# Optimization experiments

Measured on AMD Instinct MI355X. Metric: run time of the kernel, lower is better.

Reference implementation:

```python
import jax, jax.numpy as jnp
import numpy as np

# ---- static configuration (matches init_kwargs / input_specs) ----
B, N = 4, 128            # images, proposals per image
C = 256                  # feature channels (in_channels)
HF, WF = 23, 30          # feature map size (input 736x960 / 32)
PH, PW = 7, 7            # pooled_size
SCALE = 1.0 / 32.0       # scale_factor
HIMG, WIMG = HF * 32, WF * 32
KH = HF // PH + 2        # max rows any pooling bin can span
KW = WF // PW + 2        # max cols any pooling bin can span
HID, OUT = 256, 5
NEG = -1e30


def _roi_pool_one(f, box):
    """Quantized ROI max pooling for one proposal.
    f: (C, HF, WF) feature map; box: (4,) [x1,y1,x2,y2] in feature coords.
    Returns (C, PH, PW)."""
    box = jax.lax.stop_gradient(box)  # indices are non-differentiable
    x1 = jnp.clip(jnp.floor(box[0]).astype(jnp.int32), 0, WF - 1)
    y1 = jnp.clip(jnp.floor(box[1]).astype(jnp.int32), 0, HF - 1)
    roi_w = jnp.clip(jnp.ceil(box[2]).astype(jnp.int32) - x1, 1, WF)
    roi_h = jnp.clip(jnp.ceil(box[3]).astype(jnp.int32) - y1, 1, HF)
    ph = jnp.arange(PH)
    pw = jnp.arange(PW)
    hs = y1 + (ph * roi_h) // PH                       # bin row starts (PH,)
    he = y1 + ((ph + 1) * roi_h + PH - 1) // PH        # bin row ends (ceil)
    ws = x1 + (pw * roi_w) // PW
    we = x1 + ((pw + 1) * roi_w + PW - 1) // PW
    hidx = hs[:, None] + jnp.arange(KH)[None, :]       # (PH, KH)
    hval = (hidx < he[:, None]) & (hidx < HF)
    widx = ws[:, None] + jnp.arange(KW)[None, :]       # (PW, KW)
    wval = (widx < we[:, None]) & (widx < WF)
    rows = f[:, jnp.clip(hidx, 0, HF - 1), :]          # (C, PH, KH, WF) gather
    rmax = jnp.max(jnp.where(hval[None, :, :, None], rows, NEG), axis=2)  # (C, PH, WF)
    cols = rmax[:, :, jnp.clip(widx, 0, WF - 1)]       # (C, PH, PW, KW) gather
    return jnp.max(jnp.where(wval[None, None], cols, NEG), axis=3)        # (C, PH, PW)


# vmap over proposals, then over images: (B,C,HF,WF),(B,N,4) -> (B,N,C,PH,PW)
_roi_pool = jax.vmap(jax.vmap(_roi_pool_one, in_axes=(None, 0)), in_axes=(0, 0))


def setup_inputs() -> dict:
    key = jax.random.key(0)
    ks = jax.random.split(key, 8)
    features = jax.random.normal(ks[0], (B, C, HF, WF), jnp.float32)
    # valid proposals in image coordinates (min box side ~32 px)
    x1 = jax.random.uniform(ks[1], (B, N)) * (WIMG - 32.0)
    y1 = jax.random.uniform(ks[2], (B, N)) * (HIMG - 32.0)
    x2 = x1 + 32.0 + jax.random.uniform(ks[3], (B, N)) * (WIMG - 32.0 - x1)
    y2 = y1 + 32.0 + jax.random.uniform(ks[4], (B, N)) * (HIMG - 32.0 - y1)
    conf = jax.random.normal(ks[5], (B, N))
    proposals = jnp.stack([x1, y1, x2, y2, conf], axis=-1)  # (B, N, 5)
    W1 = jax.random.normal(ks[6], (HID, C * PH * PW), jnp.float32) * 0.01
    b1 = jnp.zeros((HID,), jnp.float32)
    W2 = jax.random.normal(ks[7], (OUT, HID), jnp.float32) * 0.01
    b2 = jnp.zeros((OUT,), jnp.float32)
    return {"features": features, "proposals": proposals,
            "W1": W1, "b1": b1, "W2": W2, "b2": b2}


def reference(features, proposals, W1, b1, W2, b2):
    boxes_feat = proposals[..., :4] * SCALE                 # image -> feature coords
    pooled = _roi_pool(features, boxes_feat)                # (B, N, C, PH, PW)
    flat = pooled.reshape(B, N, C * PH * PW)
    h = jax.nn.relu(jnp.einsum('bnf,hf->bnh', flat, W1) + b1)
    out = jnp.einsum('bnh,oh->bno', h, W2) + b2             # (B, N, 5)
    refined_boxes = proposals[..., :4] + out[..., :4]
    refined_conf = jax.nn.sigmoid(proposals[..., 4:5] + out[..., 4:5])
    return jnp.concatenate([refined_boxes, refined_conf], axis=-1)  # (B, N, 5)
```

## Files before the change

### kernel.cpp

```cpp
#include <hip/hip_runtime.h>
#include <math.h>

#define Bq 4
#define Nq 128
#define Cq 256
#define HFq 23
#define WFq 30
#define PHq 7
#define PWq 7
#define HIDq 256
#define OUTq 5
#define Fq (Cq*PHq*PWq)
#define Mq (Bq*Nq)
#define HWq (HFq*WFq)
#define SCALEq (1.0f/32.0f)
#define NEGq (-1e30f)
#define KHq 5
#define KWq 6
#define SPLITK 14
#define KCH (Fq/SPLITK)
#define KSTEPS (KCH/32)

typedef float f32x4 __attribute__((ext_vector_type(4)));
typedef __bf16 bf16x8 __attribute__((ext_vector_type(8)));

__device__ __forceinline__ unsigned short f2b(float f) {
    unsigned int u = __float_as_uint(f);
    unsigned int r = (u + 0x7FFFu + ((u >> 16) & 1u)) >> 16;
    return (unsigned short)r;
}

__global__ __launch_bounds__(256) void k_transpose(const float* __restrict__ feat,
                                                   float* __restrict__ ft) {
    __shared__ float t[32][33];
    int bb = blockIdx.z;
    const float* src = feat + (size_t)bb * Cq * HWq;
    float* dst = ft + (size_t)bb * HWq * Cq;
    int x0 = blockIdx.x * 32;
    int c0 = blockIdx.y * 32;
    int tx = threadIdx.x, ty = threadIdx.y;
#pragma unroll
    for (int i = 0; i < 4; ++i) {
        int c = c0 + ty + i * 8;
        int x = x0 + tx;
        if (x < HWq) t[ty + i * 8][tx] = src[(size_t)c * HWq + x];
    }
    __syncthreads();
#pragma unroll
    for (int i = 0; i < 4; ++i) {
        int x = x0 + ty + i * 8;
        int c = c0 + tx;
        if (x < HWq) dst[(size_t)x * Cq + c] = t[tx][ty + i * 8];
    }
}

__global__ __launch_bounds__(256) void k_w1perm(const float* __restrict__ W1,
                                                unsigned short* __restrict__ w1p) {
    __shared__ __align__(16) unsigned short s[Fq];
    int j = blockIdx.x;
    const float4* src = (const float4*)(W1 + (size_t)j * Fq);
    for (int i = threadIdx.x; i < Fq / 4; i += 256) {
        float4 v = src[i];
        ushort4 o;
        o.x = f2b(v.x); o.y = f2b(v.y); o.z = f2b(v.z); o.w = f2b(v.w);
        ((ushort4*)s)[i] = o;
    }
    __syncthreads();
    uint4* dst = (uint4*)(w1p + (size_t)j * Fq);
    for (int i = threadIdx.x; i < Fq / 8; i += 256) {
        int base = i * 8;
        int cell = base >> 8;
        int c0 = base & 255;
        unsigned short tmp[8];
#pragma unroll
        for (int u = 0; u < 8; ++u) tmp[u] = s[(c0 + u) * 49 + cell];
        dst[i] = *(const uint4*)tmp;
    }
}

__global__ __launch_bounds__(256) void k_pool(const float* __restrict__ ft,
                                              const float* __restrict__ props,
                                              unsigned short* __restrict__ pooled) {
    int wave = threadIdx.x >> 6;
    int lane = threadIdx.x & 63;
    int g = blockIdx.y * 4 + wave;
    int m = blockIdx.x;
    int b = m >> 7;
    const float* pr = props + (size_t)m * 5;
    float b0 = pr[0] * SCALEq, b1v = pr[1] * SCALEq;
    float b2v = pr[2] * SCALEq, b3v = pr[3] * SCALEq;
    int x1 = min(max((int)floorf(b0), 0), WFq - 1);
    int y1 = min(max((int)floorf(b1v), 0), HFq - 1);
    int rw = min(max((int)ceilf(b2v) - x1, 1), WFq);
    int rh = min(max((int)ceilf(b3v) - y1, 1), HFq);
    const float* ftb = ft + (size_t)b * HWq * Cq + lane * 4;
    unsigned short* pm = pooled + (size_t)m * Fq + lane * 4;

    for (int cell = g; cell < PHq * PWq; cell += 8) {
        int ph = cell / 7;
        int pw = cell - ph * 7;
        int hs = y1 + (ph * rh) / PHq;
        int he = min(y1 + ((ph + 1) * rh + PHq - 1) / PHq, HFq);
        int ws = x1 + (pw * rw) / PWq;
        int we = min(x1 + ((pw + 1) * rw + PWq - 1) / PWq, WFq);
        f32x4 acc = {NEGq, NEGq, NEGq, NEGq};
#pragma unroll
        for (int kh = 0; kh < KHq; ++kh) {
            if (hs + kh < he) {
                const float* rowp = ftb + (size_t)((hs + kh) * WFq) * Cq;
#pragma unroll
                for (int kw = 0; kw < KWq; ++kw) {
                    if (ws + kw < we) {
                        f32x4 v = *(const f32x4*)(rowp + (size_t)(ws + kw) * Cq);
                        acc.x = fmaxf(acc.x, v.x);
                        acc.y = fmaxf(acc.y, v.y);
                        acc.z = fmaxf(acc.z, v.z);
                        acc.w = fmaxf(acc.w, v.w);
                    }
                }
            }
        }
        ushort4 o;
        o.x = f2b(acc.x); o.y = f2b(acc.y); o.z = f2b(acc.z); o.w = f2b(acc.w);
        *(ushort4*)(pm + (size_t)cell * Cq) = o;
    }
}

__global__ __launch_bounds__(256) void k_gemm1(const unsigned short* __restrict__ pooled,
                                               const unsigned short* __restrict__ w1p,
                                               float* __restrict__ part) {
    __shared__ __align__(16) unsigned short As[64 * 32];
    __shared__ __align__(16) unsigned short Bs[64 * 32];
    int m0 = blockIdx.x * 64;
    int j0 = blockIdx.y * 64;
    int kz = blockIdx.z;
    int tid = threadIdx.x;
    int r = tid >> 2, qq = tid & 3;
    const uint4* ap = (const uint4*)(pooled + (size_t)(m0 + r) * Fq + (size_t)kz * KCH + qq * 8);
    const uint4* bp = (const uint4*)(w1p + (size_t)(j0 + r) * Fq + (size_t)kz * KCH + qq * 8);
    int lane = tid & 63, wv = tid >> 6;
    int q = lane >> 4, mr = lane & 15;
    f32x4 acc0 = {0.f, 0.f, 0.f, 0.f};
    f32x4 acc1 = {0.f, 0.f, 0.f, 0.f};
    f32x4 acc2 = {0.f, 0.f, 0.f, 0.f};
    f32x4 acc3 = {0.f, 0.f, 0.f, 0.f};
    const bf16x8* afp = (const bf16x8*)(As + (wv * 16 + mr) * 32 + q * 8);
    const bf16x8* bfp0 = (const bf16x8*)(Bs + (0 + mr) * 32 + q * 8);
    const bf16x8* bfp1 = (const bf16x8*)(Bs + (16 + mr) * 32 + q * 8);
    const bf16x8* bfp2 = (const bf16x8*)(Bs + (32 + mr) * 32 + q * 8);
    const bf16x8* bfp3 = (const bf16x8*)(Bs + (48 + mr) * 32 + q * 8);
    uint4* asw = (uint4*)(As + r * 32 + qq * 8);
    uint4* bsw = (uint4*)(Bs + r * 32 + qq * 8);
    uint4 av = ap[0];
    uint4 bv = bp[0];
    for (int s = 0; s < KSTEPS; ++s) {
        __syncthreads();
        *asw = av;
        *bsw = bv;
        __syncthreads();
        if (s + 1 < KSTEPS) {
            av = ap[(s + 1) * 4];
            bv = bp[(s + 1) * 4];
        }
        bf16x8 a = *afp;
        acc0 = __builtin_amdgcn_mfma_f32_16x16x32_bf16(a, *bfp0, acc0, 0, 0, 0);
        acc1 = __builtin_amdgcn_mfma_f32_16x16x32_bf16(a, *bfp1, acc1, 0, 0, 0);
        acc2 = __builtin_amdgcn_mfma_f32_16x16x32_bf16(a, *bfp2, acc2, 0, 0, 0);
        acc3 = __builtin_amdgcn_mfma_f32_16x16x32_bf16(a, *bfp3, acc3, 0, 0, 0);
    }
    float* pbase = part + (size_t)kz * Mq * HIDq;
    int mb = m0 + wv * 16 + q * 4;
    int jj = j0 + mr;
#pragma unroll
    for (int r2 = 0; r2 < 4; ++r2) {
        float* row = pbase + (size_t)(mb + r2) * HIDq + jj;
        row[0]  = acc0[r2];
        row[16] = acc1[r2];
        row[32] = acc2[r2];
        row[48] = acc3[r2];
    }
}

__global__ __launch_bounds__(256) void k_reduce(const float* __restrict__ part,
                                                const float* __restrict__ b1,
                                                float* __restrict__ h) {
    int m = blockIdx.x, j = threadIdx.x;
    float s = 0.f;
#pragma unroll
    for (int z = 0; z < SPLITK; ++z) s += part[((size_t)z * Mq + m) * HIDq + j];
    s += b1[j];
    h[(size_t)m * HIDq + j] = fmaxf(s, 0.f);
}

__global__ __launch_bounds__(256) void k_final(const float* __restrict__ h,
                                               const float* __restrict__ W2,
                                               const float* __restrict__ b2,
                                               const float* __restrict__ props,
                                               float* __restrict__ out) {
    __shared__ float red[OUTq][4];
    int m = blockIdx.x, j = threadIdx.x;
    float hv = h[(size_t)m * HIDq + j];
    float p[OUTq];
#pragma unroll
    for (int o = 0; o < OUTq; ++o) p[o] = hv * W2[(size_t)o * HIDq + j];
    int lane = j & 63, wid = j >> 6;
#pragma unroll
    for (int o = 0; o < OUTq; ++o) {
        float v = p[o];
        v += __shfl_xor(v, 1);
        v += __shfl_xor(v, 2);
        v += __shfl_xor(v, 4);
        v += __shfl_xor(v, 8);
        v += __shfl_xor(v, 16);
        v += __shfl_xor(v, 32);
        if (lane == 0) red[o][wid] = v;
    }
    __syncthreads();
    if (j < OUTq) {
        float s = red[j][0] + red[j][1] + red[j][2] + red[j][3] + b2[j];
        float pv = props[(size_t)m * 5 + j];
        float r;
        if (j < 4) r = pv + s;
        else r = 1.f / (1.f + expf(-(pv + s)));
        out[(size_t)m * 5 + j] = r;
    }
}

extern "C" void kernel_launch(void* const* d_in, const int* in_sizes, int n_in,
                              void* d_out, int out_size, void* d_ws, size_t ws_size,
                              hipStream_t stream) {
    const float* feat  = (const float*)d_in[0];
    const float* props = (const float*)d_in[1];
    const float* W1    = (const float*)d_in[2];
    const float* b1    = (const float*)d_in[3];
    const float* W2    = (const float*)d_in[4];
    const float* b2    = (const float*)d_in[5];
    float* out = (float*)d_out;

    char* ws = (char*)d_ws;
    float* ft              = (float*)(ws);
    unsigned short* w1p    = (unsigned short*)(ws + 2826240);
    unsigned short* pooled = (unsigned short*)(ws + 9248768);
    float* part            = (float*)(ws + 22093824);
    float* h               = (float*)(ws + 29433856);

    k_transpose<<<dim3(22, 8, 4), dim3(32, 8), 0, stream>>>(feat, ft);
    k_w1perm<<<HIDq, 256, 0, stream>>>(W1, w1p);
    k_pool<<<dim3(Mq, 2), 256, 0, stream>>>(ft, props, pooled);
    k_gemm1<<<dim3(8, 4, SPLITK), 256, 0, stream>>>(pooled, w1p, part);
    k_reduce<<<Mq, 256, 0, stream>>>(part, b1, h);
    k_final<<<Mq, 256, 0, stream>>>(h, W2, b2, props, out);
}
```

Baseline: 128.7 us.

## Fuse all stages into one cooperative persistent kernel with grid syncs

Replaces the six separate kernel launches (transpose, W1 permute, pool, split-K GEMM, reduce, final) with a single cooperative kernel of 256 blocks that runs each stage in turn and separates them with grid-wide syncs. The split-K factor drops from 14 to 8 so the GEMM tile count matches the 256-block grid, and the reduce and final stages are merged so the h buffer is no longer written. This removes launch overhead and intermediate round-trips. In exchange each stage is limited to 256 blocks, which lowers parallelism in the pool stage, and each grid sync has its own cost.

```diff
diff --git a/kernel.cpp b/kernel.cpp
--- a/kernel.cpp
+++ b/kernel.cpp
@@ -1,5 +1,8 @@
 #include <hip/hip_runtime.h>
+#include <hip/hip_cooperative_groups.h>
 #include <math.h>
+
+namespace cg = cooperative_groups;
 
 #define Bq 4
 #define Nq 128
@@ -17,7 +20,7 @@
 #define NEGq (-1e30f)
 #define KHq 5
 #define KWq 6
-#define SPLITK 14
+#define SPLITK 8
 #define KCH (Fq/SPLITK)
 #define KSTEPS (KCH/32)
 
@@ -30,199 +33,209 @@
     return (unsigned short)r;
 }
 
-__global__ __launch_bounds__(256) void k_transpose(const float* __restrict__ feat,
-                                                   float* __restrict__ ft) {
-    __shared__ float t[32][33];
-    int bb = blockIdx.z;
-    const float* src = feat + (size_t)bb * Cq * HWq;
-    float* dst = ft + (size_t)bb * HWq * Cq;
-    int x0 = blockIdx.x * 32;
-    int c0 = blockIdx.y * 32;
-    int tx = threadIdx.x, ty = threadIdx.y;
-#pragma unroll
-    for (int i = 0; i < 4; ++i) {
-        int c = c0 + ty + i * 8;
-        int x = x0 + tx;
-        if (x < HWq) t[ty + i * 8][tx] = src[(size_t)c * HWq + x];
-    }
-    __syncthreads();
-#pragma unroll
-    for (int i = 0; i < 4; ++i) {
-        int x = x0 + ty + i * 8;
-        int c = c0 + tx;
-        if (x < HWq) dst[(size_t)x * Cq + c] = t[tx][ty + i * 8];
-    }
-}
-
-__global__ __launch_bounds__(256) void k_w1perm(const float* __restrict__ W1,
-                                                unsigned short* __restrict__ w1p) {
-    __shared__ __align__(16) unsigned short s[Fq];
-    int j = blockIdx.x;
-    const float4* src = (const float4*)(W1 + (size_t)j * Fq);
-    for (int i = threadIdx.x; i < Fq / 4; i += 256) {
-        float4 v = src[i];
-        ushort4 o;
-        o.x = f2b(v.x); o.y = f2b(v.y); o.z = f2b(v.z); o.w = f2b(v.w);
-        ((ushort4*)s)[i] = o;
-    }
-    __syncthreads();
-    uint4* dst = (uint4*)(w1p + (size_t)j * Fq);
-    for (int i = threadIdx.x; i < Fq / 8; i += 256) {
-        int base = i * 8;
-        int cell = base >> 8;
-        int c0 = base & 255;
-        unsigned short tmp[8];
-#pragma unroll
-        for (int u = 0; u < 8; ++u) tmp[u] = s[(c0 + u) * 49 + cell];
-        dst[i] = *(const uint4*)tmp;
-    }
-}
-
-__global__ __launch_bounds__(256) void k_pool(const float* __restrict__ ft,
-                                              const float* __restrict__ props,
-                                              unsigned short* __restrict__ pooled) {
-    int wave = threadIdx.x >> 6;
-    int lane = threadIdx.x & 63;
-    int g = blockIdx.y * 4 + wave;
-    int m = blockIdx.x;
-    int b = m >> 7;
-    const float* pr = props + (size_t)m * 5;
-    float b0 = pr[0] * SCALEq, b1v = pr[1] * SCALEq;
-    float b2v = pr[2] * SCALEq, b3v = pr[3] * SCALEq;
-    int x1 = min(max((int)floorf(b0), 0), WFq - 1);
-    int y1 = min(max((int)floorf(b1v), 0), HFq - 1);
-    int rw = min(max((int)ceilf(b2v) - x1, 1), WFq);
-    int rh = min(max((int)ceilf(b3v) - y1, 1), HFq);
-    const float* ftb = ft + (size_t)b * HWq * Cq + lane * 4;
-    unsigned short* pm = pooled + (size_t)m * Fq + lane * 4;
-
-    for (int cell = g; cell < PHq * PWq; cell += 8) {
-        int ph = cell / 7;
-        int pw = cell - ph * 7;
-        int hs = y1 + (ph * rh) / PHq;
-        int he = min(y1 + ((ph + 1) * rh + PHq - 1) / PHq, HFq);
-        int ws = x1 + (pw * rw) / PWq;
-        int we = min(x1 + ((pw + 1) * rw + PWq - 1) / PWq, WFq);
-        f32x4 acc = {NEGq, NEGq, NEGq, NEGq};
-#pragma unroll
-        for (int kh = 0; kh < KHq; ++kh) {
-            if (hs + kh < he) {
-                const float* rowp = ftb + (size_t)((hs + kh) * WFq) * Cq;
-#pragma unroll
-                for (int kw = 0; kw < KWq; ++kw) {
-                    if (ws + kw < we) {
-                        f32x4 v = *(const f32x4*)(rowp + (size_t)(ws + kw) * Cq);
-                        acc.x = fmaxf(acc.x, v.x);
-                        acc.y = fmaxf(acc.y, v.y);
-                        acc.z = fmaxf(acc.z, v.z);
-                        acc.w = fmaxf(acc.w, v.w);
+union SMem {
+    float t[32][33];
+    unsigned short s[Fq];
+    struct { unsigned short A[64 * 32]; unsigned short B[64 * 32]; } g;
+    float red[OUTq][4];
+};
+
+__global__ __launch_bounds__(256) void k_fused(const float* __restrict__ feat,
+                                               const float* __restrict__ props,
+                                               const float* __restrict__ W1,
+                                               const float* __restrict__ b1,
+                                               const float* __restrict__ W2,
+                                               const float* __restrict__ b2,
+                                               float* __restrict__ out,
+                                               float* __restrict__ ft,
+                                               unsigned short* __restrict__ w1p,
+                                               unsigned short* __restrict__ pooled,
+                                               float* __restrict__ part) {
+    cg::grid_group grid = cg::this_grid();
+    __shared__ __align__(16) SMem sm;
+    int tid = threadIdx.x;
+    int bid = blockIdx.x;
+
+    {
+        int tx = tid & 31, ty = tid >> 5;
+        for (int job = bid; job < 704; job += 256) {
+            int bb = job / 176;
+            int rem = job - bb * 176;
+            int cblk = rem / 22;
+            int xblk = rem - cblk * 22;
+            const float* src = feat + (size_t)bb * Cq * HWq;
+            float* dst = ft + (size_t)bb * HWq * Cq;
+            int x0 = xblk * 32, c0 = cblk * 32;
+#pragma unroll
+            for (int i = 0; i < 4; ++i) {
+                int c = c0 + ty + i * 8, x = x0 + tx;
+                if (x < HWq) sm.t[ty + i * 8][tx] = src[(size_t)c * HWq + x];
+            }
+            __syncthreads();
+#pragma unroll
+            for (int i = 0; i < 4; ++i) {
+                int x = x0 + ty + i * 8, c = c0 + tx;
+                if (x < HWq) dst[(size_t)x * Cq + c] = sm.t[tx][ty + i * 8];
+            }
+            __syncthreads();
+        }
+    }
+    {
+        int j = bid;
+        const float4* src = (const float4*)(W1 + (size_t)j * Fq);
+        for (int i = tid; i < Fq / 4; i += 256) {
+            float4 v = src[i];
+            ushort4 o;
+            o.x = f2b(v.x); o.y = f2b(v.y); o.z = f2b(v.z); o.w = f2b(v.w);
+            ((ushort4*)sm.s)[i] = o;
+        }
+        __syncthreads();
+        uint4* dst = (uint4*)(w1p + (size_t)j * Fq);
+        for (int i = tid; i < Fq / 8; i += 256) {
+            int base = i * 8;
+            int cell = base >> 8;
+            int c0 = base & 255;
+            unsigned short tmp[8];
+#pragma unroll
+            for (int u = 0; u < 8; ++u) tmp[u] = sm.s[(c0 + u) * 49 + cell];
+            dst[i] = *(const uint4*)tmp;
+        }
+    }
+    grid.sync();
+    {
+        int wave = tid >> 6, lane = tid & 63;
+#pragma unroll
+        for (int rep = 0; rep < 2; ++rep) {
+            int m = bid + rep * 256;
+            const float* pr = props + (size_t)m * 5;
+            float b0 = pr[0] * SCALEq, b1v = pr[1] * SCALEq;
+            float b2v = pr[2] * SCALEq, b3v = pr[3] * SCALEq;
+            int x1 = min(max((int)floorf(b0), 0), WFq - 1);
+            int y1 = min(max((int)floorf(b1v), 0), HFq - 1);
+            int rw = min(max((int)ceilf(b2v) - x1, 1), WFq);
+            int rh = min(max((int)ceilf(b3v) - y1, 1), HFq);
+            const float* ftb = ft + (size_t)(m >> 7) * HWq * Cq + lane * 4;
+            unsigned short* pm = pooled + (size_t)m * Fq + lane * 4;
+            for (int cell = wave; cell < PHq * PWq; cell += 4) {
+                int ph = cell / 7;
+                int pw = cell - ph * 7;
+                int hs = y1 + (ph * rh) / PHq;
+                int he = min(y1 + ((ph + 1) * rh + PHq - 1) / PHq, HFq);
+                int wss = x1 + (pw * rw) / PWq;
+                int wee = min(x1 + ((pw + 1) * rw + PWq - 1) / PWq, WFq);
+                f32x4 acc = {NEGq, NEGq, NEGq, NEGq};
+#pragma unroll
+                for (int kh = 0; kh < KHq; ++kh) {
+                    if (hs + kh < he) {
+                        const float* rowp = ftb + (size_t)((hs + kh) * WFq) * Cq;
+#pragma unroll
+                        for (int kw = 0; kw < KWq; ++kw) {
+                            if (wss + kw < wee) {
+                                f32x4 v = *(const f32x4*)(rowp + (size_t)(wss + kw) * Cq);
+                                acc.x = fmaxf(acc.x, v.x);
+                                acc.y = fmaxf(acc.y, v.y);
+                                acc.z = fmaxf(acc.z, v.z);
+                                acc.w = fmaxf(acc.w, v.w);
+                            }
+                        }
                     }
                 }
-            }
-        }
-        ushort4 o;
-        o.x = f2b(acc.x); o.y = f2b(acc.y); o.z = f2b(acc.z); o.w = f2b(acc.w);
-        *(ushort4*)(pm + (size_t)cell * Cq) = o;
-    }
-}
-
-__global__ __launch_bounds__(256) void k_gemm1(const unsigned short* __restrict__ pooled,
-                                               const unsigned short* __restrict__ w1p,
-                                               float* __restrict__ part) {
-    __shared__ __align__(16) unsigned short As[64 * 32];
-    __shared__ __align__(16) unsigned short Bs[64 * 32];
-    int m0 = blockIdx.x * 64;
-    int j0 = blockIdx.y * 64;
-    int kz = blockIdx.z;
-    int tid = threadIdx.x;
-    int r = tid >> 2, qq = tid & 3;
-    const uint4* ap = (const uint4*)(pooled + (size_t)(m0 + r) * Fq + (size_t)kz * KCH + qq * 8);
-    const uint4* bp = (const uint4*)(w1p + (size_t)(j0 + r) * Fq + (size_t)kz * KCH + qq * 8);
-    int lane = tid & 63, wv = tid >> 6;
-    int q = lane >> 4, mr = lane & 15;
-    f32x4 acc0 = {0.f, 0.f, 0.f, 0.f};
-    f32x4 acc1 = {0.f, 0.f, 0.f, 0.f};
-    f32x4 acc2 = {0.f, 0.f, 0.f, 0.f};
-    f32x4 acc3 = {0.f, 0.f, 0.f, 0.f};
-    const bf16x8* afp = (const bf16x8*)(As + (wv * 16 + mr) * 32 + q * 8);
-    const bf16x8* bfp0 = (const bf16x8*)(Bs + (0 + mr) * 32 + q * 8);
-    const bf16x8* bfp1 = (const bf16x8*)(Bs + (16 + mr) * 32 + q * 8);
-    const bf16x8* bfp2 = (const bf16x8*)(Bs + (32 + mr) * 32 + q * 8);
-    const bf16x8* bfp3 = (const bf16x8*)(Bs + (48 + mr) * 32 + q * 8);
-    uint4* asw = (uint4*)(As + r * 32 + qq * 8);
-    uint4* bsw = (uint4*)(Bs + r * 32 + qq * 8);
-    uint4 av = ap[0];
-    uint4 bv = bp[0];
-    for (int s = 0; s < KSTEPS; ++s) {
-        __syncthreads();
-        *asw = av;
-        *bsw = bv;
-        __syncthreads();
-        if (s + 1 < KSTEPS) {
-            av = ap[(s + 1) * 4];
-            bv = bp[(s + 1) * 4];
-        }
-        bf16x8 a = *afp;
-        acc0 = __builtin_amdgcn_mfma_f32_16x16x32_bf16(a, *bfp0, acc0, 0, 0, 0);
-        acc1 = __builtin_amdgcn_mfma_f32_16x16x32_bf16(a, *bfp1, acc1, 0, 0, 0);
-        acc2 = __builtin_amdgcn_mfma_f32_16x16x32_bf16(a, *bfp2, acc2, 0, 0, 0);
-        acc3 = __builtin_amdgcn_mfma_f32_16x16x32_bf16(a, *bfp3, acc3, 0, 0, 0);
-    }
-    float* pbase = part + (size_t)kz * Mq * HIDq;
-    int mb = m0 + wv * 16 + q * 4;
-    int jj = j0 + mr;
-#pragma unroll
-    for (int r2 = 0; r2 < 4; ++r2) {
-        float* row = pbase + (size_t)(mb + r2) * HIDq + jj;
-        row[0]  = acc0[r2];
-        row[16] = acc1[r2];
-        row[32] = acc2[r2];
-        row[48] = acc3[r2];
-    }
-}
-
-__global__ __launch_bounds__(256) void k_reduce(const float* __restrict__ part,
-                                                const float* __restrict__ b1,
-                                                float* __restrict__ h) {
-    int m = blockIdx.x, j = threadIdx.x;
-    float s = 0.f;
-#pragma unroll
-    for (int z = 0; z < SPLITK; ++z) s += part[((size_t)z * Mq + m) * HIDq + j];
-    s += b1[j];
-    h[(size_t)m * HIDq + j] = fmaxf(s, 0.f);
-}
-
-__global__ __launch_bounds__(256) void k_final(const float* __restrict__ h,
-                                               const float* __restrict__ W2,
-                                               const float* __restrict__ b2,
-                                               const float* __restrict__ props,
-                                               float* __restrict__ out) {
-    __shared__ float red[OUTq][4];
-    int m = blockIdx.x, j = threadIdx.x;
-    float hv = h[(size_t)m * HIDq + j];
-    float p[OUTq];
-#pragma unroll
-    for (int o = 0; o < OUTq; ++o) p[o] = hv * W2[(size_t)o * HIDq + j];
-    int lane = j & 63, wid = j >> 6;
-#pragma unroll
-    for (int o = 0; o < OUTq; ++o) {
-        float v = p[o];
-        v += __shfl_xor(v, 1);
-        v += __shfl_xor(v, 2);
-        v += __shfl_xor(v, 4);
-        v += __shfl_xor(v, 8);
-        v += __shfl_xor(v, 16);
-        v += __shfl_xor(v, 32);
-        if (lane == 0) red[o][wid] = v;
-    }
-    __syncthreads();
-    if (j < OUTq) {
-        float s = red[j][0] + red[j][1] + red[j][2] + red[j][3] + b2[j];
-        float pv = props[(size_t)m * 5 + j];
-        float r;
-        if (j < 4) r = pv + s;
-        else r = 1.f / (1.f + expf(-(pv + s)));
-        out[(size_t)m * 5 + j] = r;
+                ushort4 o;
+                o.x = f2b(acc.x); o.y = f2b(acc.y); o.z = f2b(acc.z); o.w = f2b(acc.w);
+                *(ushort4*)(pm + (size_t)cell * Cq) = o;
+            }
+        }
+    }
+    grid.sync();
+    {
+        int kz = bid >> 5;
+        int tile = bid & 31;
+        int m0 = (tile >> 2) * 64;
+        int j0 = (tile & 3) * 64;
+        unsigned short* As = sm.g.A;
+        unsigned short* Bs = sm.g.B;
+        int r = tid >> 2, qq = tid & 3;
+        const uint4* ap = (const uint4*)(pooled + (size_t)(m0 + r) * Fq + (size_t)kz * KCH + qq * 8);
+        const uint4* bp = (const uint4*)(w1p + (size_t)(j0 + r) * Fq + (size_t)kz * KCH + qq * 8);
+        int lane = tid & 63, wv = tid >> 6;
+        int q = lane >> 4, mr = lane & 15;
+        f32x4 acc0 = {0.f, 0.f, 0.f, 0.f};
+        f32x4 acc1 = {0.f, 0.f, 0.f, 0.f};
+        f32x4 acc2 = {0.f, 0.f, 0.f, 0.f};
+        f32x4 acc3 = {0.f, 0.f, 0.f, 0.f};
+        const bf16x8* afp = (const bf16x8*)(As + (wv * 16 + mr) * 32 + q * 8);
+        const bf16x8* bfp0 = (const bf16x8*)(Bs + (0 + mr) * 32 + q * 8);
+        const bf16x8* bfp1 = (const bf16x8*)(Bs + (16 + mr) * 32 + q * 8);
+        const bf16x8* bfp2 = (const bf16x8*)(Bs + (32 + mr) * 32 + q * 8);
+        const bf16x8* bfp3 = (const bf16x8*)(Bs + (48 + mr) * 32 + q * 8);
+        uint4* asw = (uint4*)(As + r * 32 + qq * 8);
+        uint4* bsw = (uint4*)(Bs + r * 32 + qq * 8);
+        uint4 av = ap[0];
+        uint4 bv = bp[0];
+        for (int s = 0; s < KSTEPS; ++s) {
+            __syncthreads();
+            *asw = av;
+            *bsw = bv;
+            __syncthreads();
+            if (s + 1 < KSTEPS) {
+                av = ap[(s + 1) * 4];
+                bv = bp[(s + 1) * 4];
+            }
+            bf16x8 a = *afp;
+            acc0 = __builtin_amdgcn_mfma_f32_16x16x32_bf16(a, *bfp0, acc0, 0, 0, 0);
+            acc1 = __builtin_amdgcn_mfma_f32_16x16x32_bf16(a, *bfp1, acc1, 0, 0, 0);
+            acc2 = __builtin_amdgcn_mfma_f32_16x16x32_bf16(a, *bfp2, acc2, 0, 0, 0);
+            acc3 = __builtin_amdgcn_mfma_f32_16x16x32_bf16(a, *bfp3, acc3, 0, 0, 0);
+        }
+        float* pbase = part + (size_t)kz * Mq * HIDq;
+        int mb = m0 + wv * 16 + q * 4;
+        int jj = j0 + mr;
+#pragma unroll
+        for (int r2 = 0; r2 < 4; ++r2) {
+            float* row = pbase + (size_t)(mb + r2) * HIDq + jj;
+            row[0]  = acc0[r2];
+            row[16] = acc1[r2];
+            row[32] = acc2[r2];
+            row[48] = acc3[r2];
+        }
+    }
+    grid.sync();
+    {
+        int j = tid;
+        int lane = tid & 63, wid = tid >> 6;
+#pragma unroll
+        for (int rep = 0; rep < 2; ++rep) {
+            int m = bid + rep * 256;
+            float s = 0.f;
+#pragma unroll
+            for (int z = 0; z < SPLITK; ++z) s += part[((size_t)z * Mq + m) * HIDq + j];
+            s += b1[j];
+            float hv = fmaxf(s, 0.f);
+            float p[OUTq];
+#pragma unroll
+            for (int o = 0; o < OUTq; ++o) p[o] = hv * W2[(size_t)o * HIDq + j];
+#pragma unroll
+            for (int o = 0; o < OUTq; ++o) {
+                float v = p[o];
+                v += __shfl_xor(v, 1);
+                v += __shfl_xor(v, 2);
+                v += __shfl_xor(v, 4);
+                v += __shfl_xor(v, 8);
+                v += __shfl_xor(v, 16);
+                v += __shfl_xor(v, 32);
+                if (lane == 0) sm.red[o][wid] = v;
+            }
+            __syncthreads();
+            if (j < OUTq) {
+                float sv = sm.red[j][0] + sm.red[j][1] + sm.red[j][2] + sm.red[j][3] + b2[j];
+                float pv = props[(size_t)m * 5 + j];
+                float r;
+                if (j < 4) r = pv + sv;
+                else r = 1.f / (1.f + expf(-(pv + sv)));
+                out[(size_t)m * 5 + j] = r;
+            }
+            __syncthreads();
+        }
     }
 }
 
@@ -242,12 +255,10 @@
     unsigned short* w1p    = (unsigned short*)(ws + 2826240);
     unsigned short* pooled = (unsigned short*)(ws + 9248768);
     float* part            = (float*)(ws + 22093824);
-    float* h               = (float*)(ws + 29433856);
-
-    k_transpose<<<dim3(22, 8, 4), dim3(32, 8), 0, stream>>>(feat, ft);
-    k_w1perm<<<HIDq, 256, 0, stream>>>(W1, w1p);
-    k_pool<<<dim3(Mq, 2), 256, 0, stream>>>(ft, props, pooled);
-    k_gemm1<<<dim3(8, 4, SPLITK), 256, 0, stream>>>(pooled, w1p, part);
-    k_reduce<<<Mq, 256, 0, stream>>>(part, b1, h);
-    k_final<<<Mq, 256, 0, stream>>>(h, W2, b2, props, out);
+
+    void* args[] = {(void*)&feat, (void*)&props, (void*)&W1, (void*)&b1,
+                    (void*)&W2, (void*)&b2, (void*)&out,
+                    (void*)&ft, (void*)&w1p, (void*)&pooled, (void*)&part};
+    hipLaunchCooperativeKernel((const void*)k_fused, dim3(256), dim3(256),
+                               args, 0, stream);
 }
```

Measured after the change: 270.4 us. +110.1%, slower.
